# Optimization experiments

Hardware: AMD Instinct MI355X
Metric: run time of the kernel (lower is better)

## Reference

```python
import jax, jax.numpy as jnp
import numpy as np


def setup_inputs() -> dict:
    key = jax.random.key(0)
    ks = jax.random.split(key, 14)
    B, Ld, Lq, D = 64, 512, 128, 512
    d_node = jax.random.normal(ks[0], (B, Ld, D), jnp.float32)
    q_node = jax.random.normal(ks[1], (B, Lq, D), jnp.float32)
    qq_graph = jax.random.randint(ks[2], (B, Lq, Lq), 0, 2, jnp.int32)
    dq_graph = jax.random.randint(ks[3], (B, Ld, Lq), 0, 2, jnp.int32)
    dd_graph = jax.random.randint(ks[4], (B, Ld, Ld), 0, 2, jnp.int32)
    qd_graph = jax.random.randint(ks[5], (B, Lq, Ld), 0, 2, jnp.int32)
    s = 0.02
    W_nw = jax.random.normal(ks[6], (1, D), jnp.float32) * s
    b_nw = jnp.zeros((1,), jnp.float32)
    W_self = jax.random.normal(ks[7], (D, D), jnp.float32) * s
    b_self = jnp.zeros((D,), jnp.float32)
    W_dd = jax.random.normal(ks[8], (D, D), jnp.float32) * s
    W_qq = jax.random.normal(ks[9], (D, D), jnp.float32) * s
    W_dq = jax.random.normal(ks[10], (D, D), jnp.float32) * s
    W_qd = jax.random.normal(ks[11], (D, D), jnp.float32) * s
    return {"d_node": d_node, "q_node": q_node, "qq_graph": qq_graph,
            "dq_graph": dq_graph, "dd_graph": dd_graph, "qd_graph": qd_graph,
            "W_nw": W_nw, "b_nw": b_nw, "W_self": W_self, "b_self": b_self,
            "W_dd": W_dd, "W_qq": W_qq, "W_dq": W_dq, "W_qd": W_qd,
            "iteration_steps": 2}


def reference(d_node, q_node, qq_graph, dq_graph, dd_graph, qd_graph,
              W_nw, b_nw, W_self, b_self, W_dd, W_qq, W_dq, W_qd,
              iteration_steps):
    dd = dd_graph.astype(jnp.float32)
    dq = dq_graph.astype(jnp.float32)
    qq = qq_graph.astype(jnp.float32)
    qd = qd_graph.astype(jnp.float32)

    # neighbor counts, clamped to 1 where a node has no neighbors
    d_nb = dd.sum(-1) + dq.sum(-1)              # [B, Ld]
    d_nb = jnp.where(d_nb >= 1.0, d_nb, 1.0)
    q_nb = qq.sum(-1) + qd.sum(-1)              # [B, Lq]
    q_nb = jnp.where(q_nb >= 1.0, q_nb, 1.0)

    all_d_w, all_q_w = [], []
    for _ in range(iteration_steps):
        d_w = jax.nn.sigmoid(jnp.einsum('bld,od->blo', d_node, W_nw) + b_nw)[..., 0]  # [B, Ld]
        q_w = jax.nn.sigmoid(jnp.einsum('bld,od->blo', q_node, W_nw) + b_nw)[..., 0]  # [B, Lq]
        all_d_w.append(d_w)
        all_q_w.append(q_w)

        self_d = jnp.einsum('bld,od->blo', d_node, W_self) + b_self
        self_q = jnp.einsum('bld,od->blo', q_node, W_self) + b_self
        dd_info = jnp.einsum('bld,od->blo', d_node, W_dd)
        qd_info = jnp.einsum('bld,od->blo', d_node, W_qd)
        qq_info = jnp.einsum('bld,od->blo', q_node, W_qq)
        dq_info = jnp.einsum('bld,od->blo', q_node, W_dq)

        # masked weights: graph is 0/1, so replace_masked_values(., graph, 0) == graph * weight
        dd_msg = jnp.einsum('bij,bjd->bid', dd * d_w[:, None, :], dd_info)  # [B,Ld,D]
        qd_msg = jnp.einsum('bij,bjd->bid', qd * d_w[:, None, :], qd_info)  # [B,Lq,D]
        qq_msg = jnp.einsum('bij,bjd->bid', qq * q_w[:, None, :], qq_info)  # [B,Lq,D]
        dq_msg = jnp.einsum('bij,bjd->bid', dq * q_w[:, None, :], dq_info)  # [B,Ld,D]

        agg_q = (qq_msg + qd_msg) / q_nb[..., None]
        agg_d = (dd_msg + dq_msg) / d_nb[..., None]
        d_node = jax.nn.relu(self_d + agg_d)
        q_node = jax.nn.relu(self_q + agg_q)

    all_d_w = jnp.stack(all_d_w, axis=1)  # [B, steps, Ld]
    all_q_w = jnp.stack(all_q_w, axis=1)  # [B, steps, Lq]
    return (d_node, q_node, all_d_w, all_q_w)
```

## Files before the change

### kernel.cpp

```cpp
#include <hip/hip_runtime.h>
#include <cstdint>
#include <cstddef>

typedef _Float16 h16;
typedef __attribute__((ext_vector_type(8))) _Float16 h16x8;
typedef __attribute__((ext_vector_type(4))) _Float16 h16x4;
typedef __attribute__((ext_vector_type(4))) float f32x4;

constexpr int B_ = 64, LD = 512, LQ = 128, DIM = 512, STEPS = 2;
constexpr int MD = B_ * LD;
constexpr int MQ = B_ * LQ;
constexpr int KST = LD + LQ;
constexpr int KAGG = KST + DIM;

#define ASYNC16(gp, lp)                                                          \
  __builtin_amdgcn_global_load_lds(                                              \
      (const __attribute__((address_space(1))) unsigned int*)(gp),               \
      (__attribute__((address_space(3))) unsigned int*)(lp), 16, 0, 0)

struct Src {
  const h16* p0; int s0; long bstr0;
  const h16* p1; int s1; long bstr1;
  int ksplit;
};

template <int BM, class Epi>
__device__ __forceinline__ void gemm_body(int b, long tileM, long tileN,
                                          Src sa, Src sb, int K,
                                          const Epi& epi, h16* lds) {
  constexpr int AE = BM * 32;
  constexpr int BUFE = AE + 256 * 32;
  constexpr int NA = BM / 128;

  const int tid = threadIdx.x;
  const int lane = tid & 63;
  const int wv = tid >> 6;
  const int wr = (BM == 256) ? (wv >> 2) : 0;
  const int wc = wv & 3;
  const int quad = lane >> 4, l16 = lane & 15;

  const int u = tid & 255;
  const int sb2 = tid >> 8;
  const int r = u >> 2;
  const int es = (r ^ (r >> 2)) & 3;
  const int kq = (u & 3) ^ es;

  const h16* pa[2][NA];
  const h16* pb[2][2];
#pragma unroll
  for (int s = 0; s < NA; s++) {
    const long row = tileM + sb2 * 64 + r + 128 * s;
    pa[0][s] = sa.p0 + (size_t)b * sa.bstr0 + row * (long)sa.s0 + kq * 8;
    pa[1][s] = sa.p1 + (size_t)b * sa.bstr1 + row * (long)sa.s1 + kq * 8 - sa.ksplit;
  }
#pragma unroll
  for (int s = 0; s < 2; s++) {
    const long row = tileN + sb2 * 64 + r + 128 * s;
    pb[0][s] = sb.p0 + (size_t)b * sb.bstr0 + row * (long)sb.s0 + kq * 8;
    pb[1][s] = sb.p1 + (size_t)b * sb.bstr1 + row * (long)sb.s1 + kq * 8 - sb.ksplit;
  }

  const int ef = (l16 ^ (l16 >> 2)) & 3;
  int offA[8], offB[4];
#pragma unroll
  for (int i = 0; i < 8; i++) {
    const int row = wr * 128 + i * 16 + l16;
    offA[i] = (row * 4 + (quad ^ ef)) * 8;
  }
#pragma unroll
  for (int j = 0; j < 4; j++) {
    const int row = wc * 64 + j * 16 + l16;
    offB[j] = AE + (row * 4 + (quad ^ ef)) * 8;
  }

  f32x4 acc[8][4] = {};
  const int T = K >> 5;

  auto dmaTile = [&](int t, int off) {
    const int k0 = t * 32;
    h16* base = lds + off + tid * 8;
    const int sel = (k0 >= sa.ksplit);
#pragma unroll
    for (int s = 0; s < NA; s++) ASYNC16(pa[sel][s] + k0, base + 4096 * s);
    const int selb = (k0 >= sb.ksplit);
#pragma unroll
    for (int s = 0; s < 2; s++) ASYNC16(pb[selb][s] + k0, base + AE + 4096 * s);
  };
  auto mfmaStep = [&](int off) {
    h16x8 af[8], bf[4];
#pragma unroll
    for (int i = 0; i < 8; i++) af[i] = *(const h16x8*)(lds + off + offA[i]);
#pragma unroll
    for (int j = 0; j < 4; j++) bf[j] = *(const h16x8*)(lds + off + offB[j]);
#pragma unroll
    for (int i = 0; i < 8; i++)
#pragma unroll
      for (int j = 0; j < 4; j++)
        acc[i][j] = __builtin_amdgcn_mfma_f32_16x16x32_f16(af[i], bf[j], acc[i][j], 0, 0, 0);
  };

  dmaTile(0, 0);
  dmaTile(1, BUFE);

  int co = 0;
  int no = 2 * BUFE;
  for (int t = 0; t < T - 1; ++t) {
    if constexpr (NA == 2) asm volatile("s_waitcnt vmcnt(4)" ::: "memory");
    else                   asm volatile("s_waitcnt vmcnt(3)" ::: "memory");
    __builtin_amdgcn_s_barrier();
    asm volatile("" ::: "memory");
    __builtin_amdgcn_sched_barrier(0);
    if (t + 2 < T) dmaTile(t + 2, no);
    mfmaStep(co);
    co = (co == 2 * BUFE) ? 0 : co + BUFE;
    no = (no == 2 * BUFE) ? 0 : no + BUFE;
  }
  asm volatile("s_waitcnt vmcnt(0)" ::: "memory");
  __builtin_amdgcn_s_barrier();
  asm volatile("" ::: "memory");
  __builtin_amdgcn_sched_barrier(0);
  mfmaStep(co);

#pragma unroll
  for (int i = 0; i < 8; i++) {
#pragma unroll
    for (int j = 0; j < 4; j++) {
      const int gm0 = (int)tileM + wr * 128 + i * 16 + quad * 4;
      const int gn  = (int)tileN + wc * 64 + j * 16 + l16;
#pragma unroll
      for (int rr = 0; rr < 4; rr++) epi(b, gm0 + rr, gn, acc[i][j][rr]);
    }
  }
}

struct EpiDense {
  const float* w;
  h16* stackA;
  h16* stackB;
  int lnShift;
  int offA, offB;
  __device__ void operator()(int, int gm, int gn, float v) const {
    const int b = gn >> lnShift, l = gn & ((1 << lnShift) - 1);
    const h16 sv = (h16)(w[gn] * v);
    if (gm < 512)
      stackA[((size_t)b * 512 + gm) * 640 + offA + l] = sv;
    else
      stackB[((size_t)b * 512 + (gm - 512)) * 640 + offB + l] = sv;
  }
};
struct EpiAgg {
  const float* bias;
  float* out;
  h16* nodeNext;
  int rowsPerB;
  __device__ void operator()(int b, int gm, int gn, float v) const {
    const size_t row = (size_t)b * rowsPerB + gm;
    const float val = fmaxf(v + bias[gn], 0.f);
    if (out) out[row * 512 + gn] = val;
    if (nodeNext) nodeNext[row * 512 + gn] = (h16)val;
  }
};

__global__ __launch_bounds__(512, 2) void k_dense(Src saD, Src sbD, EpiDense epiD,
                                                  Src saQ, Src sbQ, EpiDense epiQ) {
  __shared__ __align__(16) h16 lds[3 * (256 * 32 + 256 * 32)];
  const int g = blockIdx.x;
  const int x = g / 160;
  const int yy = g % 160;
  if (yy < 128)
    gemm_body<256>(0, (long)x * 256, (long)yy * 256, saD, sbD, 512, epiD, lds);
  else
    gemm_body<256>(0, (long)x * 256, (long)(yy - 128) * 256, saQ, sbQ, 512, epiQ, lds);
}

__global__ __launch_bounds__(512, 2) void k_agg(Src saD, Src sbD, EpiAgg epiD,
                                                Src saQ, Src sbQ, EpiAgg epiQ) {
  __shared__ __align__(16) h16 lds[3 * (256 * 32 + 256 * 32)];
  const int g = blockIdx.x;
  const int b = g & 63;
  const int inner = g >> 6;
  if (inner >= 2) {
    const int i2 = inner - 2;
    gemm_body<256>(b, (long)(i2 >> 1) * 256, (long)(i2 & 1) * 256, saD, sbD, KAGG, epiD, lds);
  } else {
    gemm_body<128>(b, 0L, (long)inner * 256, saQ, sbQ, KAGG, epiQ, lds);
  }
}

__global__ __launch_bounds__(256) void k_convert(const float* __restrict__ dn,
                                                 const float* __restrict__ qn,
                                                 h16* __restrict__ dnb,
                                                 h16* __restrict__ qnb) {
  const size_t i4 = ((size_t)blockIdx.x * 256 + threadIdx.x) * 4;
  constexpr size_t TD = (size_t)MD * DIM;
  const float* src; h16* dst; size_t idx;
  if (i4 < TD) { src = dn; dst = dnb; idx = i4; }
  else         { src = qn; dst = qnb; idx = i4 - TD; }
  const float4 v = *(const float4*)&src[idx];
  h16x4 o; o.x = (h16)v.x; o.y = (h16)v.y; o.z = (h16)v.z; o.w = (h16)v.w;
  *(h16x4*)&dst[idx] = o;
}

__global__ __launch_bounds__(256) void k_wcat(const float* __restrict__ Wself,
                                              const float* __restrict__ Wdd,
                                              const float* __restrict__ Wqd,
                                              const float* __restrict__ Wqq,
                                              const float* __restrict__ Wdq,
                                              h16* __restrict__ catD,
                                              h16* __restrict__ catQ) {
  const int i = blockIdx.x * 256 + threadIdx.x;
  float vD, vQ;
  if (i < 512 * 512)       { vD = Wself[i];            vQ = vD; }
  else if (i < 1024 * 512) { vD = Wdd[i - 512 * 512];  vQ = Wqq[i - 512 * 512]; }
  else                     { vD = Wqd[i - 1024 * 512]; vQ = Wdq[i - 1024 * 512]; }
  catD[i] = (h16)vD; catQ[i] = (h16)vQ;
}

__global__ __launch_bounds__(256) void k_maskD(const int* __restrict__ dd,
                                               const int* __restrict__ dq,
                                               h16* __restrict__ maskD) {
  const int row = blockIdx.x * 4 + (threadIdx.x >> 6);
  const int lane = threadIdx.x & 63;
  const int* pdd = dd + (size_t)row * 512;
  const int* pdq = dq + (size_t)row * 128;
  h16* pm = maskD + (size_t)row * 640;
  float vals[10];
  float s = 0.f;
#pragma unroll
  for (int t = 0; t < 10; t++) {
    const int j = lane + t * 64;
    const float v = (float)((j < 512) ? pdd[j] : pdq[j - 512]);
    vals[t] = v; s += v;
  }
  for (int m = 32; m; m >>= 1) s += __shfl_xor(s, m);
  const float inv = 1.f / fmaxf(s, 1.f);
#pragma unroll
  for (int t = 0; t < 10; t++) pm[lane + t * 64] = (h16)(vals[t] * inv);
}

__global__ __launch_bounds__(256) void k_maskQ(const int* __restrict__ qq,
                                               const int* __restrict__ qd,
                                               h16* __restrict__ maskQ) {
  const int row = blockIdx.x * 4 + (threadIdx.x >> 6);
  const int lane = threadIdx.x & 63;
  const int* pqq = qq + (size_t)row * 128;
  const int* pqd = qd + (size_t)row * 512;
  h16* pm = maskQ + (size_t)row * 640;
  float vals[10];
  float s = 0.f;
#pragma unroll
  for (int t = 0; t < 10; t++) {
    const int j = lane + t * 64;
    const float v = (float)((j < 128) ? pqq[j] : pqd[j - 128]);
    vals[t] = v; s += v;
  }
  for (int m = 32; m; m >>= 1) s += __shfl_xor(s, m);
  const float inv = 1.f / fmaxf(s, 1.f);
#pragma unroll
  for (int t = 0; t < 10; t++) pm[lane + t * 64] = (h16)(vals[t] * inv);
}

__global__ __launch_bounds__(256) void k_w(const h16* __restrict__ dnb,
                                           const h16* __restrict__ qnb,
                                           const float* __restrict__ Wnw,
                                           const float* __restrict__ bnw,
                                           float* __restrict__ d_w,
                                           float* __restrict__ q_w,
                                           float* __restrict__ adw,
                                           float* __restrict__ aqw, int it) {
  const int row = blockIdx.x * 4 + (threadIdx.x >> 6);
  const int lane = threadIdx.x & 63;
  const bool isD = row < MD;
  const h16* node = isD ? dnb + (size_t)row * 512 : qnb + (size_t)(row - MD) * 512;
  const h16x8 v = *(const h16x8*)&node[lane * 8];
  const float4 w0 = *(const float4*)&Wnw[lane * 8];
  const float4 w1 = *(const float4*)&Wnw[lane * 8 + 4];
  float s = (float)v[0] * w0.x + (float)v[1] * w0.y + (float)v[2] * w0.z +
            (float)v[3] * w0.w + (float)v[4] * w1.x + (float)v[5] * w1.y +
            (float)v[6] * w1.z + (float)v[7] * w1.w;
  for (int m = 32; m; m >>= 1) s += __shfl_xor(s, m);
  if (lane == 0) {
    const float w = 1.f / (1.f + expf(-(s + bnw[0])));
    if (isD) {
      d_w[row] = w;
      adw[((size_t)(row >> 9) * STEPS + it) * 512 + (row & 511)] = w;
    } else {
      const int rq = row - MD;
      q_w[rq] = w;
      aqw[((size_t)(rq >> 7) * STEPS + it) * 128 + (rq & 127)] = w;
    }
  }
}

extern "C" void kernel_launch(void* const* d_in, const int* in_sizes, int n_in,
                              void* d_out, int out_size, void* d_ws, size_t ws_size,
                              hipStream_t stream) {
  (void)in_sizes; (void)n_in; (void)out_size; (void)ws_size;

  const float* d_node = (const float*)d_in[0];
  const float* q_node = (const float*)d_in[1];
  const int*   qq     = (const int*)d_in[2];
  const int*   dq     = (const int*)d_in[3];
  const int*   dd     = (const int*)d_in[4];
  const int*   qd     = (const int*)d_in[5];
  const float* W_nw   = (const float*)d_in[6];
  const float* b_nw   = (const float*)d_in[7];
  const float* W_self = (const float*)d_in[8];
  const float* b_self = (const float*)d_in[9];
  const float* W_dd   = (const float*)d_in[10];
  const float* W_qq   = (const float*)d_in[11];
  const float* W_dq   = (const float*)d_in[12];
  const float* W_qd   = (const float*)d_in[13];

  float* outd = (float*)d_out;
  float* outq = outd + (size_t)MD * DIM;
  float* adw  = outq + (size_t)MQ * DIM;
  float* aqw  = adw + (size_t)B_ * STEPS * LD;

  char* p = (char*)d_ws;
  auto alloc = [&](size_t bytes) { char* r = p; p += (bytes + 255) & ~(size_t)255; return r; };
  h16* dnode[2], *qnode[2];
  dnode[0] = (h16*)alloc((size_t)MD * DIM * 2);
  dnode[1] = (h16*)alloc((size_t)MD * DIM * 2);
  qnode[0] = (h16*)alloc((size_t)MQ * DIM * 2);
  qnode[1] = (h16*)alloc((size_t)MQ * DIM * 2);
  h16* catD    = (h16*)alloc((size_t)1536 * 512 * 2);
  h16* catQ    = (h16*)alloc((size_t)1536 * 512 * 2);
  h16* maskD   = (h16*)alloc((size_t)B_ * LD * KST * 2);
  h16* maskQ   = (h16*)alloc((size_t)B_ * LQ * KST * 2);
  h16* stackDT = (h16*)alloc((size_t)B_ * 512 * KST * 2);
  h16* stackQT = (h16*)alloc((size_t)B_ * 512 * KST * 2);
  float* d_wb  = (float*)alloc((size_t)MD * 4);
  float* q_wb  = (float*)alloc((size_t)MQ * 4);

  k_convert<<<dim3((MD * DIM + MQ * DIM) / 4 / 256), 256, 0, stream>>>(d_node, q_node, dnode[0], qnode[0]);
  k_wcat<<<dim3(1536 * 512 / 256), 256, 0, stream>>>(W_self, W_dd, W_qd, W_qq, W_dq, catD, catQ);
  k_maskD<<<dim3(MD / 4), 256, 0, stream>>>(dd, dq, maskD);
  k_maskQ<<<dim3(MQ / 4), 256, 0, stream>>>(qq, qd, maskQ);

  for (int it = 0; it < STEPS; it++) {
    const bool last = (it == STEPS - 1);
    h16* ncur_d = dnode[it & 1];
    h16* nnext_d = dnode[(it & 1) ^ 1];
    h16* ncur_q = qnode[it & 1];
    h16* nnext_q = qnode[(it & 1) ^ 1];

    k_w<<<dim3((MD + MQ) / 4), 256, 0, stream>>>(ncur_d, ncur_q, W_nw, b_nw, d_wb, q_wb, adw, aqw, it);

    {
      Src saD{catD + 512 * 512, 512, 0, catD + 512 * 512, 512, 0, 512};
      Src sbD{ncur_d, 512, 0, ncur_d, 512, 0, 512};
      Src saQ{catQ + 512 * 512, 512, 0, catQ + 512 * 512, 512, 0, 512};
      Src sbQ{ncur_q, 512, 0, ncur_q, 512, 0, 512};
      k_dense<<<dim3(640), 512, 0, stream>>>(
          saD, sbD, EpiDense{d_wb, stackDT, stackQT, 9, 0, 128},
          saQ, sbQ, EpiDense{q_wb, stackQT, stackDT, 7, 0, 512});
    }
    {
      Src saD{maskD, 640, (long)LD * KST, ncur_d, 512, (long)LD * DIM, KST};
      Src sbD{stackDT, 640, (long)512 * KST, catD, 512, 0, KST};
      Src saQ{maskQ, 640, (long)LQ * KST, ncur_q, 512, (long)LQ * DIM, KST};
      Src sbQ{stackQT, 640, (long)512 * KST, catQ, 512, 0, KST};
      k_agg<<<dim3(384), 512, 0, stream>>>(
          saD, sbD, EpiAgg{b_self, last ? outd : nullptr, last ? nullptr : nnext_d, 512},
          saQ, sbQ, EpiAgg{b_self, last ? outq : nullptr, last ? nullptr : nnext_q, 128});
    }
  }
}
```

Baseline: 620.1 us.

## Split GEMM main loop into two phases with setprio and retile Q agg

The shared GEMM body is templated on per-wave M/N fragment counts. Each k-step is split into two halves: A and B DMA issues are interleaved between them, with an extra barrier, and s_setprio is raised around the MFMA bursts. The Q-side aggregation now uses 128x128 tiles instead of 128x256, raising the k_agg grid from 384 to 512 blocks for better CU fill. The cost is an extra barrier per k-step and a waitcnt schedule that depends on the load count.

```diff
diff --git a/kernel.cpp b/kernel.cpp
--- a/kernel.cpp
+++ b/kernel.cpp
@@ -24,19 +24,23 @@
   int ksplit;
 };
 
-template <int BM, class Epi>
+template <int WM, int WN, class Epi>
 __device__ __forceinline__ void gemm_body(int b, long tileM, long tileN,
                                           Src sa, Src sb, int K,
                                           const Epi& epi, h16* lds) {
+  constexpr int BM = WM * 32;
+  constexpr int BN = WN * 64;
   constexpr int AE = BM * 32;
-  constexpr int BUFE = AE + 256 * 32;
+  constexpr int BUFE = (BM + BN) * 32;
   constexpr int NA = BM / 128;
+  constexpr int NB = BN / 128;
+  constexpr int LT = NA + NB;
+  constexpr int HM = WM / 2;
 
   const int tid = threadIdx.x;
   const int lane = tid & 63;
   const int wv = tid >> 6;
-  const int wr = (BM == 256) ? (wv >> 2) : 0;
-  const int wc = wv & 3;
+  const int wr = wv >> 2, wc = wv & 3;
   const int quad = lane >> 4, l16 = lane & 15;
 
   const int u = tid & 255;
@@ -46,7 +50,7 @@
   const int kq = (u & 3) ^ es;
 
   const h16* pa[2][NA];
-  const h16* pb[2][2];
+  const h16* pb[2][NB];
 #pragma unroll
   for (int s = 0; s < NA; s++) {
     const long row = tileM + sb2 * 64 + r + 128 * s;
@@ -54,64 +58,89 @@
     pa[1][s] = sa.p1 + (size_t)b * sa.bstr1 + row * (long)sa.s1 + kq * 8 - sa.ksplit;
   }
 #pragma unroll
-  for (int s = 0; s < 2; s++) {
+  for (int s = 0; s < NB; s++) {
     const long row = tileN + sb2 * 64 + r + 128 * s;
     pb[0][s] = sb.p0 + (size_t)b * sb.bstr0 + row * (long)sb.s0 + kq * 8;
     pb[1][s] = sb.p1 + (size_t)b * sb.bstr1 + row * (long)sb.s1 + kq * 8 - sb.ksplit;
   }
 
   const int ef = (l16 ^ (l16 >> 2)) & 3;
-  int offA[8], offB[4];
-#pragma unroll
-  for (int i = 0; i < 8; i++) {
-    const int row = wr * 128 + i * 16 + l16;
+  int offA[WM], offB[WN];
+#pragma unroll
+  for (int i = 0; i < WM; i++) {
+    const int row = wr * (WM * 16) + i * 16 + l16;
     offA[i] = (row * 4 + (quad ^ ef)) * 8;
   }
 #pragma unroll
-  for (int j = 0; j < 4; j++) {
-    const int row = wc * 64 + j * 16 + l16;
+  for (int j = 0; j < WN; j++) {
+    const int row = wc * (WN * 16) + j * 16 + l16;
     offB[j] = AE + (row * 4 + (quad ^ ef)) * 8;
   }
 
-  f32x4 acc[8][4] = {};
+  f32x4 acc[WM][WN] = {};
   const int T = K >> 5;
 
-  auto dmaTile = [&](int t, int off) {
+  auto dmaA = [&](int t, int off) {
     const int k0 = t * 32;
     h16* base = lds + off + tid * 8;
     const int sel = (k0 >= sa.ksplit);
 #pragma unroll
     for (int s = 0; s < NA; s++) ASYNC16(pa[sel][s] + k0, base + 4096 * s);
-    const int selb = (k0 >= sb.ksplit);
-#pragma unroll
-    for (int s = 0; s < 2; s++) ASYNC16(pb[selb][s] + k0, base + AE + 4096 * s);
   };
-  auto mfmaStep = [&](int off) {
-    h16x8 af[8], bf[4];
-#pragma unroll
-    for (int i = 0; i < 8; i++) af[i] = *(const h16x8*)(lds + off + offA[i]);
-#pragma unroll
-    for (int j = 0; j < 4; j++) bf[j] = *(const h16x8*)(lds + off + offB[j]);
-#pragma unroll
-    for (int i = 0; i < 8; i++)
-#pragma unroll
-      for (int j = 0; j < 4; j++)
+  auto dmaB = [&](int t, int off) {
+    const int k0 = t * 32;
+    h16* base = lds + off + AE + tid * 8;
+    const int sel = (k0 >= sb.ksplit);
+#pragma unroll
+    for (int s = 0; s < NB; s++) ASYNC16(pb[sel][s] + k0, base + 4096 * s);
+  };
+
+  h16x8 bf[WN];
+  auto phase0 = [&](int off) {
+    h16x8 af[HM];
+#pragma unroll
+    for (int j = 0; j < WN; j++) bf[j] = *(const h16x8*)(lds + off + offB[j]);
+#pragma unroll
+    for (int i = 0; i < HM; i++) af[i] = *(const h16x8*)(lds + off + offA[i]);
+    __builtin_amdgcn_s_setprio(1);
+#pragma unroll
+    for (int i = 0; i < HM; i++)
+#pragma unroll
+      for (int j = 0; j < WN; j++)
         acc[i][j] = __builtin_amdgcn_mfma_f32_16x16x32_f16(af[i], bf[j], acc[i][j], 0, 0, 0);
+    __builtin_amdgcn_s_setprio(0);
   };
-
-  dmaTile(0, 0);
-  dmaTile(1, BUFE);
+  auto phase1 = [&](int off) {
+    h16x8 af[WM - HM];
+#pragma unroll
+    for (int i = 0; i < WM - HM; i++) af[i] = *(const h16x8*)(lds + off + offA[HM + i]);
+    __builtin_amdgcn_s_setprio(1);
+#pragma unroll
+    for (int i = 0; i < WM - HM; i++)
+#pragma unroll
+      for (int j = 0; j < WN; j++)
+        acc[HM + i][j] = __builtin_amdgcn_mfma_f32_16x16x32_f16(af[i], bf[j], acc[HM + i][j], 0, 0, 0);
+    __builtin_amdgcn_s_setprio(0);
+  };
+
+  dmaA(0, 0); dmaB(0, 0);
+  dmaA(1, BUFE); dmaB(1, BUFE);
 
   int co = 0;
   int no = 2 * BUFE;
   for (int t = 0; t < T - 1; ++t) {
-    if constexpr (NA == 2) asm volatile("s_waitcnt vmcnt(4)" ::: "memory");
-    else                   asm volatile("s_waitcnt vmcnt(3)" ::: "memory");
+    if constexpr (LT == 4) asm volatile("s_waitcnt vmcnt(4)" ::: "memory");
+    else                   asm volatile("s_waitcnt vmcnt(2)" ::: "memory");
     __builtin_amdgcn_s_barrier();
     asm volatile("" ::: "memory");
     __builtin_amdgcn_sched_barrier(0);
-    if (t + 2 < T) dmaTile(t + 2, no);
-    mfmaStep(co);
+    if (t + 2 < T) dmaA(t + 2, no);
+    phase0(co);
+    __builtin_amdgcn_s_barrier();
+    asm volatile("" ::: "memory");
+    __builtin_amdgcn_sched_barrier(0);
+    if (t + 2 < T) dmaB(t + 2, no);
+    phase1(co);
     co = (co == 2 * BUFE) ? 0 : co + BUFE;
     no = (no == 2 * BUFE) ? 0 : no + BUFE;
   }
@@ -119,14 +148,18 @@
   __builtin_amdgcn_s_barrier();
   asm volatile("" ::: "memory");
   __builtin_amdgcn_sched_barrier(0);
-  mfmaStep(co);
-
-#pragma unroll
-  for (int i = 0; i < 8; i++) {
-#pragma unroll
-    for (int j = 0; j < 4; j++) {
-      const int gm0 = (int)tileM + wr * 128 + i * 16 + quad * 4;
-      const int gn  = (int)tileN + wc * 64 + j * 16 + l16;
+  phase0(co);
+  __builtin_amdgcn_s_barrier();
+  asm volatile("" ::: "memory");
+  __builtin_amdgcn_sched_barrier(0);
+  phase1(co);
+
+#pragma unroll
+  for (int i = 0; i < WM; i++) {
+#pragma unroll
+    for (int j = 0; j < WN; j++) {
+      const int gm0 = (int)tileM + wr * (WM * 16) + i * 16 + quad * 4;
+      const int gn  = (int)tileN + wc * (WN * 16) + j * 16 + l16;
 #pragma unroll
       for (int rr = 0; rr < 4; rr++) epi(b, gm0 + rr, gn, acc[i][j][rr]);
     }
@@ -168,9 +201,9 @@
   const int x = g / 160;
   const int yy = g % 160;
   if (yy < 128)
-    gemm_body<256>(0, (long)x * 256, (long)yy * 256, saD, sbD, 512, epiD, lds);
+    gemm_body<8, 4>(0, (long)x * 256, (long)yy * 256, saD, sbD, 512, epiD, lds);
   else
-    gemm_body<256>(0, (long)x * 256, (long)(yy - 128) * 256, saQ, sbQ, 512, epiQ, lds);
+    gemm_body<8, 4>(0, (long)x * 256, (long)(yy - 128) * 256, saQ, sbQ, 512, epiQ, lds);
 }
 
 __global__ __launch_bounds__(512, 2) void k_agg(Src saD, Src sbD, EpiAgg epiD,
@@ -178,13 +211,11 @@
   __shared__ __align__(16) h16 lds[3 * (256 * 32 + 256 * 32)];
   const int g = blockIdx.x;
   const int b = g & 63;
-  const int inner = g >> 6;
-  if (inner >= 2) {
-    const int i2 = inner - 2;
-    gemm_body<256>(b, (long)(i2 >> 1) * 256, (long)(i2 & 1) * 256, saD, sbD, KAGG, epiD, lds);
-  } else {
-    gemm_body<128>(b, 0L, (long)inner * 256, saQ, sbQ, KAGG, epiQ, lds);
-  }
+  const int unit = g >> 6;
+  if (unit < 4)
+    gemm_body<8, 4>(b, (long)(unit >> 1) * 256, (long)(unit & 1) * 256, saD, sbD, KAGG, epiD, lds);
+  else
+    gemm_body<4, 2>(b, 0L, (long)(unit - 4) * 128, saQ, sbQ, KAGG, epiQ, lds);
 }
 
 __global__ __launch_bounds__(256) void k_convert(const float* __restrict__ dn,
@@ -361,7 +392,7 @@
       Src sbD{stackDT, 640, (long)512 * KST, catD, 512, 0, KST};
       Src saQ{maskQ, 640, (long)LQ * KST, ncur_q, 512, (long)LQ * DIM, KST};
       Src sbQ{stackQT, 640, (long)512 * KST, catQ, 512, 0, KST};
-      k_agg<<<dim3(384), 512, 0, stream>>>(
+      k_agg<<<dim3(512), 512, 0, stream>>>(
           saD, sbD, EpiAgg{b_self, last ? outd : nullptr, last ? nullptr : nnext_d, 512},
           saQ, sbQ, EpiAgg{b_self, last ? outq : nullptr, last ? nullptr : nnext_q, 128});
     }
```

Measured after the change: 569.0 us. 1.09x faster.
